# Kernel tuning notes

Measured on AMD Instinct MI355X. Metric: run time of the kernel, lower is better.

The kernel has to match this reference:

```python
import jax, jax.numpy as jnp
import numpy as np


def setup_inputs() -> dict:
    key = jax.random.key(0)
    ks = jax.random.split(key, 8)
    B, N, D, H = 8, 512, 64, 64
    user_embeddings = jax.random.normal(ks[0], (B, N, D), dtype=jnp.float32)
    past_lengths = jax.random.randint(ks[1], (B,), 0, N)
    valid_mask = jnp.ones((B, N), dtype=jnp.float32)
    # MLP params: Linear(4D -> H), PReLU (single slope), Linear(H -> 1)
    s1 = 1.0 / np.sqrt(4 * D)
    s2 = 1.0 / np.sqrt(H)
    W1 = jax.random.uniform(ks[2], (H, 4 * D), minval=-s1, maxval=s1, dtype=jnp.float32)
    b1 = jax.random.uniform(ks[3], (H,), minval=-s1, maxval=s1, dtype=jnp.float32)
    prelu_a = jnp.float32(0.25)
    W2 = jax.random.uniform(ks[4], (1, H), minval=-s2, maxval=s2, dtype=jnp.float32)
    b2 = jax.random.uniform(ks[5], (1,), minval=-s2, maxval=s2, dtype=jnp.float32)
    return {"past_lengths": past_lengths, "user_embeddings": user_embeddings,
            "valid_mask": valid_mask, "W1": W1, "b1": b1, "prelu_a": prelu_a,
            "W2": W2, "b2": b2}


def reference(past_lengths, user_embeddings, valid_mask, W1, b1, prelu_a, W2, b2):
    # DIN local activation attention with causal mask.
    # Original math: h = W1 @ concat(Q, K, Q-K, Q*K) + b1 per (q,k) pair.
    # Split W1 into its 4 D-sized blocks so the concat tensor [B,N,N,4D] is
    # never materialized; the pairwise hidden [B,N,N,H] is the only big buffer.
    B, N, D = user_embeddings.shape
    Wq, Wk, Wd, Wm = jnp.split(W1, 4, axis=1)  # each [H, D]
    x = user_embeddings
    # Q and (Q-K)'s +Q part -> per-query term; K and (Q-K)'s -K part -> per-key term
    hq = jnp.einsum('bqd,hd->bqh', x, Wq + Wd)          # [B,N,H]
    hk = jnp.einsum('bkd,hd->bkh', x, Wk - Wd)          # [B,N,H]
    hm = jnp.einsum('bqd,bkd,hd->bqkh', x, x, Wm)       # [B,N,N,H] (Q*K term)
    h = hq[:, :, None, :] + hk[:, None, :, :] + hm + b1
    h = jnp.where(h > 0, h, prelu_a * h)                # PReLU
    scores = jnp.einsum('bqkh,h->bqk', h, W2[0]) + b2[0]  # [B,N,N]
    causal = jnp.tril(jnp.ones((N, N), dtype=scores.dtype))
    scores = scores * causal[None, :, :]
    scores = scores * valid_mask[:, None, :]            # key-side padding mask
    encoded = jnp.einsum('bqk,bkd->bqd', scores, x)     # weighted sum (no softmax)
    return encoded
```

## Files before the change

kernel.cpp:

```cpp
#include <hip/hip_runtime.h>

#define NB 8
#define NN 512

#define WS_WMF 0
#define WS_HQ  4096
#define WS_BF  266240
#define WS_XE  528384

typedef float fx4 __attribute__((ext_vector_type(4)));
typedef short sx8 __attribute__((ext_vector_type(8)));
typedef int   ix4 __attribute__((ext_vector_type(4)));

static __device__ inline unsigned short f2bf(float f) {
    unsigned u = __float_as_uint(f);
    return (unsigned short)((u + 0x7FFFu + ((u >> 16) & 1u)) >> 16);
}

__global__ __launch_bounds__(256) void prep(const float* __restrict__ x,
                                            const float* __restrict__ vm,
                                            const float* __restrict__ W1,
                                            const float* __restrict__ b1,
                                            float* __restrict__ ws) {
    __shared__ float lwq[64 * 65];
    __shared__ float lwk[64 * 65];
    __shared__ float xs[256];
    const int t = threadIdx.x;
    const int blk = blockIdx.x;

    {
        int d = t & 63, hb = t >> 6;
        #pragma unroll 4
        for (int i = 0; i < 16; ++i) {
            int h = i * 4 + hb;
            float a = W1[h * 256 + d];
            float bb = W1[h * 256 + 64 + d];
            float c = W1[h * 256 + 128 + d];
            lwq[d * 65 + h] = a + c;
            lwk[d * 65 + h] = bb - c;
        }
    }
    const int r0 = blk * 4;
    xs[t] = x[r0 * 64 + t];
    __syncthreads();

    {
        int r = t >> 6, h = t & 63;
        const float* xr = xs + r * 64;
        float aq = b1[h], ak = 0.f;
        #pragma unroll
        for (int dd = 0; dd < 64; ++dd) {
            float xv = xr[dd];
            aq = fmaf(xv, lwq[dd * 65 + h], aq);
            ak = fmaf(xv, lwk[dd * 65 + h], ak);
        }
        int row = r0 + r;
        (ws + WS_HQ)[row * 64 + h] = aq;
        unsigned short* bfp = (unsigned short*)(ws + WS_BF);
        int bb = row >> 9, k = row & 511;
        int tt = k >> 4, nn = k & 15;
        int c = 2 + (h >> 5);
        int qd = (h >> 3) & 3, j = h & 7;
        int ln = qd * 16 + nn;
        bfp[((((bb * 32 + tt) * 4 + c) * 64 + ln) << 3) + j] = f2bf(ak);
    }

    if (blk < 256) {
        int b = blk >> 5, t5 = blk & 31;
        if (t < 128) {
            unsigned short* bfp = (unsigned short*)(ws + WS_BF);
            int c = t >> 6, L = t & 63;
            int nn = L & 15, qd = L >> 4;
            const float* src = x + ((b * 512 + t5 * 16 + nn) * 64 + c * 32 + qd * 8);
            fx4 v0 = *(const fx4*)src;
            fx4 v1 = *(const fx4*)(src + 4);
            uint4 o;
            o.x = (unsigned)f2bf(v0[0]) | ((unsigned)f2bf(v0[1]) << 16);
            o.y = (unsigned)f2bf(v0[2]) | ((unsigned)f2bf(v0[3]) << 16);
            o.z = (unsigned)f2bf(v1[0]) | ((unsigned)f2bf(v1[1]) << 16);
            o.w = (unsigned)f2bf(v1[2]) | ((unsigned)f2bf(v1[3]) << 16);
            *(uint4*)(bfp + ((((b * 32 + t5) * 4 + c) * 64 + L) << 3)) = o;
        }
        {
            unsigned short* xep = (unsigned short*)(ws + WS_XE);
            int c32 = t5 >> 1, half = t5 & 1;
            int nt = t >> 6, r = t & 63;
            int L = half * 32 + (r & 31);
            int j0 = (r >> 5) * 4;
            int quad = L >> 4, nn = L & 15;
            unsigned short u[4];
            #pragma unroll
            for (int i = 0; i < 4; ++i) {
                int key = c32 * 32 + quad * 8 + j0 + i;
                float v = x[(b * 512 + key) * 64 + nt * 16 + nn] * vm[b * 512 + key];
                u[i] = f2bf(v);
            }
            uint2 o;
            o.x = (unsigned)u[0] | ((unsigned)u[1] << 16);
            o.y = (unsigned)u[2] | ((unsigned)u[3] << 16);
            *(uint2*)(xep + (((((b * 16 + c32) * 4 + nt) * 64 + L) << 3) + j0)) = o;
        }
    } else if (blk < 258) {
        float* wmf = ws + WS_WMF;
        int e = (blk - 256) * 256 + t;
        int slot = e >> 6, lane = e & 63;
        int ht = slot >> 1, hf = slot & 1;
        int m = lane & 15, qd = lane >> 4;
        int h = ht * 16 + m;
        int dbase = hf * 32 + qd * 8;
        #pragma unroll
        for (int j = 0; j < 8; ++j)
            wmf[e * 8 + j] = W1[h * 256 + 192 + dbase + j];
    }
}

__global__ __launch_bounds__(256, 2) void k2_main(const float* __restrict__ x,
                                                  const float* __restrict__ prelu_a,
                                                  const float* __restrict__ W2,
                                                  const float* __restrict__ b2,
                                                  const float* __restrict__ ws,
                                                  float* __restrict__ out) {
    const int tid  = threadIdx.x;
    const int lane = tid & 63;
    const int w    = tid >> 6;
    const int wid  = blockIdx.x * 4 + w;
    const int b    = wid >> 9;
    const int rr   = wid & 511;
    const int q    = (rr & 1) ? (511 - (rr >> 1)) : (rr >> 1);
    const int n    = lane & 15, quad = lane >> 4;
    const int bq   = b * 512 + q;

    const float* wmf = ws + WS_WMF;
    const float* hq  = ws + WS_HQ;
    const unsigned short* bfp = (const unsigned short*)(ws + WS_BF);
    const unsigned short* xep = (const unsigned short*)(ws + WS_XE);

    const float pa  = prelu_a[0];
    const float b2v = b2[0];

    __shared__ unsigned sjoint[4 * 256];
    unsigned* myS = sjoint + w * 256;

    float hqr[4][4], w2r[4][4];
    #pragma unroll
    for (int ht = 0; ht < 4; ++ht) {
        fx4 vh = *(const fx4*)(hq + bq * 64 + ht * 16 + quad * 4);
        fx4 vw = *(const fx4*)(W2 + ht * 16 + quad * 4);
        #pragma unroll
        for (int r = 0; r < 4; ++r) { hqr[ht][r] = vh[r]; w2r[ht][r] = vw[r]; }
    }

    float xq[2][8];
    {
        const float* xp = x + bq * 64 + quad * 8;
        fx4 t0 = *(const fx4*)xp;
        fx4 t1 = *(const fx4*)(xp + 4);
        fx4 t2 = *(const fx4*)(xp + 32);
        fx4 t3 = *(const fx4*)(xp + 36);
        #pragma unroll
        for (int j = 0; j < 4; ++j) {
            xq[0][j] = t0[j]; xq[0][4 + j] = t1[j];
            xq[1][j] = t2[j]; xq[1][4 + j] = t3[j];
        }
    }

    sx8 afrag[4][2];
    #pragma unroll
    for (int ht = 0; ht < 4; ++ht)
        #pragma unroll
        for (int hf = 0; hf < 2; ++hf) {
            const float* wp = wmf + (((ht * 2 + hf) * 64 + lane) << 3);
            fx4 w0 = *(const fx4*)wp;
            fx4 w1 = *(const fx4*)(wp + 4);
            sx8 a;
            #pragma unroll
            for (int j = 0; j < 4; ++j) {
                a[j]     = (short)f2bf(w0[j] * xq[hf][j]);
                a[4 + j] = (short)f2bf(w1[j] * xq[hf][4 + j]);
            }
            afrag[ht][hf] = a;
        }

    sx8 oh[4];
    #pragma unroll
    for (int ht = 0; ht < 4; ++ht) {
        sx8 a;
        #pragma unroll
        for (int j = 0; j < 8; ++j) {
            int hp = (ht >> 1) * 32 + quad * 8 + j;
            a[j] = (hp == ht * 16 + n) ? (short)0x3F80 : (short)0;
        }
        oh[ht] = a;
    }

    const int cmax = q >> 5;

    for (int c = 0; c <= cmax; ++c) {
        const unsigned short* fb = bfp + ((((b * 32 + 2 * c) * 4) * 64 + lane) << 3);
        sx8 fa0 = *(const sx8*)(fb);
        sx8 fa1 = *(const sx8*)(fb + 512);
        sx8 fa2 = *(const sx8*)(fb + 1024);
        sx8 fa3 = *(const sx8*)(fb + 1536);
        sx8 fb0 = *(const sx8*)(fb + 2048);
        sx8 fb1 = *(const sx8*)(fb + 2560);
        sx8 fb2 = *(const sx8*)(fb + 3072);
        sx8 fb3 = *(const sx8*)(fb + 3584);

        fx4 accA[4], accB[4];
        #pragma unroll
        for (int ht = 0; ht < 4; ++ht) {
            accA[ht] = (fx4){hqr[ht][0], hqr[ht][1], hqr[ht][2], hqr[ht][3]};
            accB[ht] = accA[ht];
        }
        #pragma unroll
        for (int ht = 0; ht < 4; ++ht) {
            accA[ht] = __builtin_amdgcn_mfma_f32_16x16x32_bf16(afrag[ht][0], fa0, accA[ht], 0, 0, 0);
            accB[ht] = __builtin_amdgcn_mfma_f32_16x16x32_bf16(afrag[ht][0], fb0, accB[ht], 0, 0, 0);
        }
        #pragma unroll
        for (int ht = 0; ht < 4; ++ht) {
            accA[ht] = __builtin_amdgcn_mfma_f32_16x16x32_bf16(afrag[ht][1], fa1, accA[ht], 0, 0, 0);
            accB[ht] = __builtin_amdgcn_mfma_f32_16x16x32_bf16(afrag[ht][1], fb1, accB[ht], 0, 0, 0);
        }
        #pragma unroll
        for (int ht = 0; ht < 4; ++ht) {
            accA[ht] = __builtin_amdgcn_mfma_f32_16x16x32_bf16(oh[ht], (ht < 2) ? fa2 : fa3, accA[ht], 0, 0, 0);
            accB[ht] = __builtin_amdgcn_mfma_f32_16x16x32_bf16(oh[ht], (ht < 2) ? fb2 : fb3, accB[ht], 0, 0, 0);
        }

        float s0a = 0.f, s0b = 0.f, s1a = 0.f, s1b = 0.f;
        #pragma unroll
        for (int ht = 0; ht < 2; ++ht)
            #pragma unroll
            for (int r = 0; r < 4; ++r) {
                float za = accA[ht][r], zb = accB[ht][r];
                s0a = fmaf(w2r[ht][r], fmaxf(za, za * pa), s0a);
                s1a = fmaf(w2r[ht][r], fmaxf(zb, zb * pa), s1a);
            }
        #pragma unroll
        for (int ht = 2; ht < 4; ++ht)
            #pragma unroll
            for (int r = 0; r < 4; ++r) {
                float za = accA[ht][r], zb = accB[ht][r];
                s0b = fmaf(w2r[ht][r], fmaxf(za, za * pa), s0b);
                s1b = fmaf(w2r[ht][r], fmaxf(zb, zb * pa), s1b);
            }
        float s0 = s0a + s0b, s1 = s1a + s1b;
        s0 += __shfl_xor(s0, 16, 64);
        s0 += __shfl_xor(s0, 32, 64);
        s1 += __shfl_xor(s1, 16, 64);
        s1 += __shfl_xor(s1, 32, 64);
        int k0 = c * 32 + n;
        s0 = (k0 <= q)      ? s0 + b2v : 0.f;
        s1 = (k0 + 16 <= q) ? s1 + b2v : 0.f;

        unsigned packed = (unsigned)f2bf(s0) | ((unsigned)f2bf(s1) << 16);
        if (quad == 0) myS[c * 16 + n] = packed;
    }

    const unsigned sel = (quad < 2) ? 0x05040100u : 0x07060302u;
    fx4 eacc[4];
    #pragma unroll
    for (int nt = 0; nt < 4; ++nt) eacc[nt] = (fx4){0.f, 0.f, 0.f, 0.f};

    for (int c = 0; c <= cmax; ++c) {
        const unsigned* sp = myS + c * 16 + (quad & 1) * 8;
        uint4 wv0 = *(const uint4*)sp;
        uint4 wv1 = *(const uint4*)(sp + 4);
        ix4 sw;
        sw[0] = (int)__builtin_amdgcn_perm(wv0.y, wv0.x, sel);
        sw[1] = (int)__builtin_amdgcn_perm(wv0.w, wv0.z, sel);
        sw[2] = (int)__builtin_amdgcn_perm(wv1.y, wv1.x, sel);
        sw[3] = (int)__builtin_amdgcn_perm(wv1.w, wv1.z, sel);
        sx8 sfrag = __builtin_bit_cast(sx8, sw);

        const unsigned short* fe = xep + ((((b * 16 + c) * 4) * 64 + lane) << 3);
        sx8 e0 = *(const sx8*)(fe);
        sx8 e1 = *(const sx8*)(fe + 512);
        sx8 e2 = *(const sx8*)(fe + 1024);
        sx8 e3 = *(const sx8*)(fe + 1536);

        eacc[0] = __builtin_amdgcn_mfma_f32_16x16x32_bf16(sfrag, e0, eacc[0], 0, 0, 0);
        eacc[1] = __builtin_amdgcn_mfma_f32_16x16x32_bf16(sfrag, e1, eacc[1], 0, 0, 0);
        eacc[2] = __builtin_amdgcn_mfma_f32_16x16x32_bf16(sfrag, e2, eacc[2], 0, 0, 0);
        eacc[3] = __builtin_amdgcn_mfma_f32_16x16x32_bf16(sfrag, e3, eacc[3], 0, 0, 0);
    }

    float ov = eacc[0][0];
    if (quad == 1) ov = eacc[1][0];
    if (quad == 2) ov = eacc[2][0];
    if (quad == 3) ov = eacc[3][0];
    out[bq * 64 + quad * 16 + n] = ov;
}

extern "C" void kernel_launch(void* const* d_in, const int* in_sizes, int n_in,
                              void* d_out, int out_size, void* d_ws, size_t ws_size,
                              hipStream_t stream) {
    const float* x   = (const float*)d_in[1];
    const float* vmk = (const float*)d_in[2];
    const float* W1  = (const float*)d_in[3];
    const float* b1  = (const float*)d_in[4];
    const float* pa  = (const float*)d_in[5];
    const float* W2  = (const float*)d_in[6];
    const float* b2  = (const float*)d_in[7];
    float* ws  = (float*)d_ws;
    float* out = (float*)d_out;

    hipLaunchKernelGGL(prep, dim3(NB * NN / 4), dim3(256), 0, stream,
                       x, vmk, W1, b1, ws);
    hipLaunchKernelGGL(k2_main, dim3(NB * NN / 4), dim3(256), 0, stream,
                       x, pa, W2, b2, ws, out);
}
```

Before: 120.3 us.

## Share key tiles across 8 waves via double-buffered LDS and fuse score scoring with aggregation

```diff
diff --git a/kernel.cpp b/kernel.cpp
--- a/kernel.cpp
+++ b/kernel.cpp
@@ -114,7 +114,7 @@
     }
 }
 
-__global__ __launch_bounds__(256, 2) void k2_main(const float* __restrict__ x,
+__global__ __launch_bounds__(512, 2) void k2_main(const float* __restrict__ x,
                                                   const float* __restrict__ prelu_a,
                                                   const float* __restrict__ W2,
                                                   const float* __restrict__ b2,
@@ -123,12 +123,14 @@
     const int tid  = threadIdx.x;
     const int lane = tid & 63;
     const int w    = tid >> 6;
-    const int wid  = blockIdx.x * 4 + w;
-    const int b    = wid >> 9;
-    const int rr   = wid & 511;
-    const int q    = (rr & 1) ? (511 - (rr >> 1)) : (rr >> 1);
+    const int blk  = blockIdx.x;
+    const int b    = blk >> 6;
+    const int j    = blk & 63;
+    const int q    = (w < 4) ? (4 * j + w) : (508 - 4 * j + (w - 4));
     const int n    = lane & 15, quad = lane >> 4;
     const int bq   = b * 512 + q;
+    const int cmaxw = q >> 5;
+    const int cblk  = (511 - 4 * j) >> 5;
 
     const float* wmf = ws + WS_WMF;
     const float* hq  = ws + WS_HQ;
@@ -138,8 +140,8 @@
     const float pa  = prelu_a[0];
     const float b2v = b2[0];
 
-    __shared__ unsigned sjoint[4 * 256];
-    unsigned* myS = sjoint + w * 256;
+    __shared__ uint4 bufS[2][512];
+    __shared__ uint4 bufE[2][256];
 
     float hqr[4][4], w2r[4][4];
     #pragma unroll
@@ -158,9 +160,9 @@
         fx4 t2 = *(const fx4*)(xp + 32);
         fx4 t3 = *(const fx4*)(xp + 36);
         #pragma unroll
-        for (int j = 0; j < 4; ++j) {
-            xq[0][j] = t0[j]; xq[0][4 + j] = t1[j];
-            xq[1][j] = t2[j]; xq[1][4 + j] = t3[j];
+        for (int jj = 0; jj < 4; ++jj) {
+            xq[0][jj] = t0[jj]; xq[0][4 + jj] = t1[jj];
+            xq[1][jj] = t2[jj]; xq[1][4 + jj] = t3[jj];
         }
     }
 
@@ -174,9 +176,9 @@
             fx4 w1 = *(const fx4*)(wp + 4);
             sx8 a;
             #pragma unroll
-            for (int j = 0; j < 4; ++j) {
-                a[j]     = (short)f2bf(w0[j] * xq[hf][j]);
-                a[4 + j] = (short)f2bf(w1[j] * xq[hf][4 + j]);
+            for (int jj = 0; jj < 4; ++jj) {
+                a[jj]     = (short)f2bf(w0[jj] * xq[hf][jj]);
+                a[4 + jj] = (short)f2bf(w1[jj] * xq[hf][4 + jj]);
             }
             afrag[ht][hf] = a;
         }
@@ -186,111 +188,137 @@
     for (int ht = 0; ht < 4; ++ht) {
         sx8 a;
         #pragma unroll
-        for (int j = 0; j < 8; ++j) {
-            int hp = (ht >> 1) * 32 + quad * 8 + j;
-            a[j] = (hp == ht * 16 + n) ? (short)0x3F80 : (short)0;
+        for (int jj = 0; jj < 8; ++jj) {
+            int hp = (ht >> 1) * 32 + quad * 8 + jj;
+            a[jj] = (hp == ht * 16 + n) ? (short)0x3F80 : (short)0;
         }
         oh[ht] = a;
     }
 
-    const int cmax = q >> 5;
-
-    for (int c = 0; c <= cmax; ++c) {
-        const unsigned short* fb = bfp + ((((b * 32 + 2 * c) * 4) * 64 + lane) << 3);
-        sx8 fa0 = *(const sx8*)(fb);
-        sx8 fa1 = *(const sx8*)(fb + 512);
-        sx8 fa2 = *(const sx8*)(fb + 1024);
-        sx8 fa3 = *(const sx8*)(fb + 1536);
-        sx8 fb0 = *(const sx8*)(fb + 2048);
-        sx8 fb1 = *(const sx8*)(fb + 2560);
-        sx8 fb2 = *(const sx8*)(fb + 3072);
-        sx8 fb3 = *(const sx8*)(fb + 3584);
-
-        fx4 accA[4], accB[4];
-        #pragma unroll
-        for (int ht = 0; ht < 4; ++ht) {
-            accA[ht] = (fx4){hqr[ht][0], hqr[ht][1], hqr[ht][2], hqr[ht][3]};
-            accB[ht] = accA[ht];
-        }
-        #pragma unroll
-        for (int ht = 0; ht < 4; ++ht) {
-            accA[ht] = __builtin_amdgcn_mfma_f32_16x16x32_bf16(afrag[ht][0], fa0, accA[ht], 0, 0, 0);
-            accB[ht] = __builtin_amdgcn_mfma_f32_16x16x32_bf16(afrag[ht][0], fb0, accB[ht], 0, 0, 0);
-        }
-        #pragma unroll
-        for (int ht = 0; ht < 4; ++ht) {
-            accA[ht] = __builtin_amdgcn_mfma_f32_16x16x32_bf16(afrag[ht][1], fa1, accA[ht], 0, 0, 0);
-            accB[ht] = __builtin_amdgcn_mfma_f32_16x16x32_bf16(afrag[ht][1], fb1, accB[ht], 0, 0, 0);
-        }
-        #pragma unroll
-        for (int ht = 0; ht < 4; ++ht) {
-            accA[ht] = __builtin_amdgcn_mfma_f32_16x16x32_bf16(oh[ht], (ht < 2) ? fa2 : fa3, accA[ht], 0, 0, 0);
-            accB[ht] = __builtin_amdgcn_mfma_f32_16x16x32_bf16(oh[ht], (ht < 2) ? fb2 : fb3, accB[ht], 0, 0, 0);
-        }
-
-        float s0a = 0.f, s0b = 0.f, s1a = 0.f, s1b = 0.f;
-        #pragma unroll
-        for (int ht = 0; ht < 2; ++ht)
-            #pragma unroll
-            for (int r = 0; r < 4; ++r) {
-                float za = accA[ht][r], zb = accB[ht][r];
-                s0a = fmaf(w2r[ht][r], fmaxf(za, za * pa), s0a);
-                s1a = fmaf(w2r[ht][r], fmaxf(zb, zb * pa), s1a);
-            }
-        #pragma unroll
-        for (int ht = 2; ht < 4; ++ht)
-            #pragma unroll
-            for (int r = 0; r < 4; ++r) {
-                float za = accA[ht][r], zb = accB[ht][r];
-                s0b = fmaf(w2r[ht][r], fmaxf(za, za * pa), s0b);
-                s1b = fmaf(w2r[ht][r], fmaxf(zb, zb * pa), s1b);
-            }
-        float s0 = s0a + s0b, s1 = s1a + s1b;
-        s0 += __shfl_xor(s0, 16, 64);
-        s0 += __shfl_xor(s0, 32, 64);
-        s1 += __shfl_xor(s1, 16, 64);
-        s1 += __shfl_xor(s1, 32, 64);
-        int k0 = c * 32 + n;
-        s0 = (k0 <= q)      ? s0 + b2v : 0.f;
-        s1 = (k0 + 16 <= q) ? s1 + b2v : 0.f;
-
-        unsigned packed = (unsigned)f2bf(s0) | ((unsigned)f2bf(s1) << 16);
-        if (quad == 0) myS[c * 16 + n] = packed;
-    }
-
+    int idxs[8];
+    #pragma unroll
+    for (int jj = 0; jj < 8; ++jj) idxs[jj] = ((quad * 8 + jj) & 15) << 2;
     const unsigned sel = (quad < 2) ? 0x05040100u : 0x07060302u;
+
     fx4 eacc[4];
     #pragma unroll
     for (int nt = 0; nt < 4; ++nt) eacc[nt] = (fx4){0.f, 0.f, 0.f, 0.f};
 
-    for (int c = 0; c <= cmax; ++c) {
-        const unsigned* sp = myS + c * 16 + (quad & 1) * 8;
-        uint4 wv0 = *(const uint4*)sp;
-        uint4 wv1 = *(const uint4*)(sp + 4);
-        ix4 sw;
-        sw[0] = (int)__builtin_amdgcn_perm(wv0.y, wv0.x, sel);
-        sw[1] = (int)__builtin_amdgcn_perm(wv0.w, wv0.z, sel);
-        sw[2] = (int)__builtin_amdgcn_perm(wv1.y, wv1.x, sel);
-        sw[3] = (int)__builtin_amdgcn_perm(wv1.w, wv1.z, sel);
-        sx8 sfrag = __builtin_bit_cast(sx8, sw);
-
-        const unsigned short* fe = xep + ((((b * 16 + c) * 4) * 64 + lane) << 3);
-        sx8 e0 = *(const sx8*)(fe);
-        sx8 e1 = *(const sx8*)(fe + 512);
-        sx8 e2 = *(const sx8*)(fe + 1024);
-        sx8 e3 = *(const sx8*)(fe + 1536);
-
-        eacc[0] = __builtin_amdgcn_mfma_f32_16x16x32_bf16(sfrag, e0, eacc[0], 0, 0, 0);
-        eacc[1] = __builtin_amdgcn_mfma_f32_16x16x32_bf16(sfrag, e1, eacc[1], 0, 0, 0);
-        eacc[2] = __builtin_amdgcn_mfma_f32_16x16x32_bf16(sfrag, e2, eacc[2], 0, 0, 0);
-        eacc[3] = __builtin_amdgcn_mfma_f32_16x16x32_bf16(sfrag, e3, eacc[3], 0, 0, 0);
+    {
+        const uint4* s = (const uint4*)(bfp + (unsigned)(b * 32) * 2048);
+        bufS[0][tid] = s[tid];
+        if (tid < 256) {
+            const uint4* s2 = (const uint4*)(xep + (unsigned)(b * 16) * 2048);
+            bufE[0][tid] = s2[tid];
+        }
+    }
+    __syncthreads();
+
+    for (int c = 0; c <= cblk; ++c) {
+        uint4 st, st2;
+        if (c < cblk) {
+            int cc = c + 1;
+            st = ((const uint4*)(bfp + (unsigned)(b * 32 + 2 * cc) * 2048))[tid];
+            if (tid < 256)
+                st2 = ((const uint4*)(xep + (unsigned)(b * 16 + cc) * 2048))[tid];
+        }
+
+        if (c <= cmaxw) {
+            const unsigned short* ls = (const unsigned short*)&bufS[c & 1][0] + lane * 8;
+            sx8 fa0 = *(const sx8*)(ls);
+            sx8 fa1 = *(const sx8*)(ls + 512);
+            sx8 fa2 = *(const sx8*)(ls + 1024);
+            sx8 fa3 = *(const sx8*)(ls + 1536);
+            sx8 fb0 = *(const sx8*)(ls + 2048);
+            sx8 fb1 = *(const sx8*)(ls + 2560);
+            sx8 fb2 = *(const sx8*)(ls + 3072);
+            sx8 fb3 = *(const sx8*)(ls + 3584);
+
+            fx4 accA[4], accB[4];
+            #pragma unroll
+            for (int ht = 0; ht < 4; ++ht) {
+                accA[ht] = (fx4){hqr[ht][0], hqr[ht][1], hqr[ht][2], hqr[ht][3]};
+                accB[ht] = accA[ht];
+            }
+            #pragma unroll
+            for (int ht = 0; ht < 4; ++ht) {
+                accA[ht] = __builtin_amdgcn_mfma_f32_16x16x32_bf16(afrag[ht][0], fa0, accA[ht], 0, 0, 0);
+                accB[ht] = __builtin_amdgcn_mfma_f32_16x16x32_bf16(afrag[ht][0], fb0, accB[ht], 0, 0, 0);
+            }
+            #pragma unroll
+            for (int ht = 0; ht < 4; ++ht) {
+                accA[ht] = __builtin_amdgcn_mfma_f32_16x16x32_bf16(afrag[ht][1], fa1, accA[ht], 0, 0, 0);
+                accB[ht] = __builtin_amdgcn_mfma_f32_16x16x32_bf16(afrag[ht][1], fb1, accB[ht], 0, 0, 0);
+            }
+            #pragma unroll
+            for (int ht = 0; ht < 4; ++ht) {
+                accA[ht] = __builtin_amdgcn_mfma_f32_16x16x32_bf16(oh[ht], (ht < 2) ? fa2 : fa3, accA[ht], 0, 0, 0);
+                accB[ht] = __builtin_amdgcn_mfma_f32_16x16x32_bf16(oh[ht], (ht < 2) ? fb2 : fb3, accB[ht], 0, 0, 0);
+            }
+
+            float s0a = 0.f, s0b = 0.f, s1a = 0.f, s1b = 0.f;
+            #pragma unroll
+            for (int ht = 0; ht < 2; ++ht)
+                #pragma unroll
+                for (int r = 0; r < 4; ++r) {
+                    float za = accA[ht][r], zb = accB[ht][r];
+                    s0a = fmaf(w2r[ht][r], fmaxf(za, za * pa), s0a);
+                    s1a = fmaf(w2r[ht][r], fmaxf(zb, zb * pa), s1a);
+                }
+            #pragma unroll
+            for (int ht = 2; ht < 4; ++ht)
+                #pragma unroll
+                for (int r = 0; r < 4; ++r) {
+                    float za = accA[ht][r], zb = accB[ht][r];
+                    s0b = fmaf(w2r[ht][r], fmaxf(za, za * pa), s0b);
+                    s1b = fmaf(w2r[ht][r], fmaxf(zb, zb * pa), s1b);
+                }
+            float s0 = s0a + s0b, s1 = s1a + s1b;
+            s0 += __shfl_xor(s0, 16, 64);
+            s0 += __shfl_xor(s0, 32, 64);
+            s1 += __shfl_xor(s1, 16, 64);
+            s1 += __shfl_xor(s1, 32, 64);
+            int k0 = c * 32 + n;
+            s0 = (k0 <= q)      ? s0 + b2v : 0.f;
+            s1 = (k0 + 16 <= q) ? s1 + b2v : 0.f;
+
+            unsigned packed = (unsigned)f2bf(s0) | ((unsigned)f2bf(s1) << 16);
+            int g[8];
+            #pragma unroll
+            for (int jj = 0; jj < 8; ++jj)
+                g[jj] = __builtin_amdgcn_ds_bpermute(idxs[jj], (int)packed);
+            ix4 sw_;
+            sw_[0] = (int)__builtin_amdgcn_perm((unsigned)g[1], (unsigned)g[0], sel);
+            sw_[1] = (int)__builtin_amdgcn_perm((unsigned)g[3], (unsigned)g[2], sel);
+            sw_[2] = (int)__builtin_amdgcn_perm((unsigned)g[5], (unsigned)g[4], sel);
+            sw_[3] = (int)__builtin_amdgcn_perm((unsigned)g[7], (unsigned)g[6], sel);
+            sx8 sfrag = __builtin_bit_cast(sx8, sw_);
+
+            const unsigned short* le = (const unsigned short*)&bufE[c & 1][0] + lane * 8;
+            sx8 e0 = *(const sx8*)(le);
+            sx8 e1 = *(const sx8*)(le + 512);
+            sx8 e2 = *(const sx8*)(le + 1024);
+            sx8 e3 = *(const sx8*)(le + 1536);
+
+            eacc[0] = __builtin_amdgcn_mfma_f32_16x16x32_bf16(sfrag, e0, eacc[0], 0, 0, 0);
+            eacc[1] = __builtin_amdgcn_mfma_f32_16x16x32_bf16(sfrag, e1, eacc[1], 0, 0, 0);
+            eacc[2] = __builtin_amdgcn_mfma_f32_16x16x32_bf16(sfrag, e2, eacc[2], 0, 0, 0);
+            eacc[3] = __builtin_amdgcn_mfma_f32_16x16x32_bf16(sfrag, e3, eacc[3], 0, 0, 0);
+        }
+
+        if (c < cblk) {
+            int cc = c + 1;
+            bufS[cc & 1][tid] = st;
+            if (tid < 256) bufE[cc & 1][tid] = st2;
+        }
+        __syncthreads();
     }
 
     float ov = eacc[0][0];
     if (quad == 1) ov = eacc[1][0];
     if (quad == 2) ov = eacc[2][0];
     if (quad == 3) ov = eacc[3][0];
-    out[bq * 64 + quad * 16 + n] = ov;
+    out[bq * 64 + lane] = ov;
 }
 
 extern "C" void kernel_launch(void* const* d_in, const int* in_sizes, int n_in,
@@ -308,6 +336,6 @@
 
     hipLaunchKernelGGL(prep, dim3(NB * NN / 4), dim3(256), 0, stream,
                        x, vmk, W1, b1, ws);
-    hipLaunchKernelGGL(k2_main, dim3(NB * NN / 4), dim3(256), 0, stream,
+    hipLaunchKernelGGL(k2_main, dim3(NB * 64), dim3(512), 0, stream,
                        x, pa, W2, b2, ws, out);
 }
```

Result: faster. 108.8 us (-9.5%).
